# Kernel tuning notes

Measured on AMD Instinct MI355X. Metric: run time of the kernel, lower is better.

The kernel has to match this reference:

```python
import jax, jax.numpy as jnp
import numpy as np

HID, OUT, VOCAB, MSIZE, MDIM = 1024, 512, 1024, 262144, 128


def setup_inputs() -> dict:
    key = jax.random.key(0)
    ks = jax.random.split(key, 16)
    s = lambda i, shape, scale=0.02: jax.random.normal(ks[i], shape, dtype=jnp.float32) * scale
    return {
        "input": s(0, (1, 1, VOCAB), 1.0),
        "hidden0": s(1, (1, 1, HID), 1.0),
        "stack": s(2, (MSIZE, MDIM), 1.0),
        "W_ih": s(3, (HID, VOCAB)),
        "W_hh": s(4, (HID, HID)),
        "b_ih": s(5, (HID,)),
        "b_hh": s(6, (HID,)),
        "W_y": s(7, (OUT, HID)),
        "b_y": s(8, (OUT,)),
        "W_n": s(9, (MDIM, HID)),
        "b_n": s(10, (MDIM,)),
        "W_a": s(11, (2, HID)),
        "b_a": s(12, (2,)),
        "W_sh": s(13, (HID, MDIM)),
        "b_sh": s(14, (HID,)),
    }


def reference(input, hidden0, stack, W_ih, W_hh, b_ih, b_hh, W_y, b_y, W_n, b_n, W_a, b_a, W_sh, b_sh):
    # hidden_bar = W_sh(stack[0]).view(1,1,-1) + hidden0   -> (1,1,H)
    hidden_bar = (stack[0] @ W_sh.T + b_sh)[None, None, :] + hidden0
    # single-step, single-layer tanh RNN cell
    h = jnp.tanh(input @ W_ih.T + b_ih + hidden_bar @ W_hh.T + b_hh)  # (1,1,H)
    output = jax.nn.sigmoid(h @ W_y.T + b_y).reshape(-1, OUT)          # (1,OUT)
    action_weights = jax.nn.softmax(h @ W_a.T + b_a, axis=2).reshape(-1)  # (2,)
    new_elt = jax.nn.sigmoid(h @ W_n.T + b_n).reshape(1, MDIM)         # (1,MDIM)
    push_side = jnp.concatenate([new_elt, stack[:-1]], axis=0)
    pop_side = jnp.concatenate([stack[1:], jnp.zeros((1, MDIM), dtype=stack.dtype)], axis=0)
    new_stack = action_weights[0] * push_side + action_weights[1] * pop_side
    return output, h, new_stack
```

## Files before the change

### kernel.cpp

```cpp
#include <hip/hip_runtime.h>
#include <cmath>

#define HID 1024
#define OUTN 512
#define VOCABN 1024
#define MSIZE 262144
#define MDIM 128

#define WS_TIH 0
#define WS_HB  1024
#define WS_H   2048
#define WS_AW  3072
#define WS_NE  3076

typedef float f4_t __attribute__((ext_vector_type(4)));

__device__ __forceinline__ float wred(float v) {
#pragma unroll
    for (int m = 32; m; m >>= 1) v += __shfl_xor(v, m, 64);
    return v;
}

__device__ __forceinline__ float dot4(const float4* __restrict__ a,
                                      const float4* __restrict__ b,
                                      int n4, int lane) {
    float acc = 0.f;
    for (int k = lane; k < n4; k += 64) {
        float4 x = a[k], y = b[k];
        acc = fmaf(x.x, y.x, fmaf(x.y, y.y, fmaf(x.z, y.z, fmaf(x.w, y.w, acc))));
    }
    return wred(acc);
}

__global__ void k_pre(const float* __restrict__ input, const float* __restrict__ hidden0,
                      const float* __restrict__ stack, const float* __restrict__ W_ih,
                      const float* __restrict__ b_ih, const float* __restrict__ W_sh,
                      const float* __restrict__ b_sh, float* __restrict__ ws) {
    const int lane = threadIdx.x & 63;
    const int row = blockIdx.x * (blockDim.x >> 6) + (threadIdx.x >> 6);
    if (row >= HID) return;
    float t  = dot4((const float4*)(W_ih + row * VOCABN), (const float4*)input, VOCABN / 4, lane);
    float hb = dot4((const float4*)(W_sh + row * MDIM), (const float4*)stack, MDIM / 4, lane);
    if (lane == 0) {
        ws[WS_TIH + row] = t + b_ih[row];
        ws[WS_HB + row]  = hb + b_sh[row] + hidden0[row];
    }
}

__global__ void k_h(const float* __restrict__ W_hh, const float* __restrict__ b_hh,
                    float* __restrict__ ws, float* __restrict__ d_out) {
    const int lane = threadIdx.x & 63;
    const int row = blockIdx.x * (blockDim.x >> 6) + (threadIdx.x >> 6);
    if (row >= HID) return;
    float a = dot4((const float4*)(W_hh + row * HID), (const float4*)(ws + WS_HB), HID / 4, lane);
    if (lane == 0) {
        float h = tanhf(ws[WS_TIH + row] + a + b_hh[row]);
        ws[WS_H + row] = h;
        d_out[OUTN + row] = h;
    }
}

__global__ void k_heads(const float* __restrict__ W_y, const float* __restrict__ b_y,
                        const float* __restrict__ W_n, const float* __restrict__ b_n,
                        const float* __restrict__ W_a, const float* __restrict__ b_a,
                        float* __restrict__ ws, float* __restrict__ d_out) {
    const int lane = threadIdx.x & 63;
    const int row = blockIdx.x * (blockDim.x >> 6) + (threadIdx.x >> 6);
    const float4* h4 = (const float4*)(ws + WS_H);
    if (row < OUTN) {
        float a = dot4((const float4*)(W_y + row * HID), h4, HID / 4, lane);
        if (lane == 0) d_out[row] = 1.f / (1.f + expf(-(a + b_y[row])));
    } else if (row < OUTN + MDIM) {
        const int m = row - OUTN;
        float a = dot4((const float4*)(W_n + m * HID), h4, HID / 4, lane);
        if (lane == 0) ws[WS_NE + m] = 1.f / (1.f + expf(-(a + b_n[m])));
    } else if (row == OUTN + MDIM) {
        float l0 = dot4((const float4*)(W_a), h4, HID / 4, lane);
        float l1 = dot4((const float4*)(W_a + HID), h4, HID / 4, lane);
        if (lane == 0) {
            l0 += b_a[0];
            l1 += b_a[1];
            const float mx = fmaxf(l0, l1);
            const float e0 = expf(l0 - mx), e1 = expf(l1 - mx);
            const float s = e0 + e1;
            ws[WS_AW]     = e0 / s;
            ws[WS_AW + 1] = e1 / s;
        }
    }
}

__global__ __launch_bounds__(256, 8) void k_stack(
    const float* __restrict__ stack, const float* __restrict__ ws,
    float* __restrict__ out_stack) {
    const float aw0 = ws[WS_AW];
    const float aw1 = ws[WS_AW + 1];
    const float4* s4  = (const float4*)stack;
    const float4* ne4 = (const float4*)(ws + WS_NE);
    f4_t* o4 = (f4_t*)out_stack;
    const int total4 = MSIZE * (MDIM / 4);
    const int lane = threadIdx.x & 63;
    const int wid  = blockIdx.x * 4 + (threadIdx.x >> 6);
    const long base = (long)wid * 1024;

    float4 prev;
    if (wid == 0) prev = (lane < 32) ? ne4[lane] : s4[lane - 32];
    else          prev = s4[base - 32 + lane];

#pragma unroll 4
    for (int i = 0; i < 16; ++i) {
        const long A = base + i * 64;
        const long nidx = A + 32 + lane;
        float4 next = make_float4(0.f, 0.f, 0.f, 0.f);
        if (nidx < total4) next = s4[nidx];
        f4_t r;
        r.x = fmaf(aw0, prev.x, aw1 * next.x);
        r.y = fmaf(aw0, prev.y, aw1 * next.y);
        r.z = fmaf(aw0, prev.z, aw1 * next.z);
        r.w = fmaf(aw0, prev.w, aw1 * next.w);
        __builtin_nontemporal_store(r, &o4[A + lane]);
        prev = next;
    }
}

extern "C" void kernel_launch(void* const* d_in, const int* in_sizes, int n_in,
                              void* d_out, int out_size, void* d_ws, size_t ws_size,
                              hipStream_t stream) {
    const float* input   = (const float*)d_in[0];
    const float* hidden0 = (const float*)d_in[1];
    const float* stack   = (const float*)d_in[2];
    const float* W_ih    = (const float*)d_in[3];
    const float* W_hh    = (const float*)d_in[4];
    const float* b_ih    = (const float*)d_in[5];
    const float* b_hh    = (const float*)d_in[6];
    const float* W_y     = (const float*)d_in[7];
    const float* b_y     = (const float*)d_in[8];
    const float* W_n     = (const float*)d_in[9];
    const float* b_n     = (const float*)d_in[10];
    const float* W_a     = (const float*)d_in[11];
    const float* b_a     = (const float*)d_in[12];
    const float* W_sh    = (const float*)d_in[13];
    const float* b_sh    = (const float*)d_in[14];
    float* out = (float*)d_out;
    float* ws  = (float*)d_ws;

    k_pre<<<256, 256, 0, stream>>>(input, hidden0, stack, W_ih, b_ih, W_sh, b_sh, ws);
    k_h<<<256, 256, 0, stream>>>(W_hh, b_hh, ws, out);
    k_heads<<<161, 256, 0, stream>>>(W_y, b_y, W_n, b_n, W_a, b_a, ws, out);
    k_stack<<<2048, 256, 0, stream>>>(stack, ws, out + OUTN + HID);
}
```

Measured before the change: 60.09 us.

## Fuse RNN matvec chain into one cooperative kernel with grid syncs

Merges the three dependent matvec kernels (pre-activation, hidden update, output heads) into one cooperative kernel launched with 256 blocks. Grid-wide barriers replace the kernel boundaries between stages. The aim is to cut two launch gaps and kernel drain/fill overhead. In exchange it adds cooperative-launch overhead and grid-sync cost, and still needs a separate stack kernel.

Measured after the change: 118.0 us. 1.96x slower.

```diff
diff --git a/kernel.cpp b/kernel.cpp
--- a/kernel.cpp
+++ b/kernel.cpp
@@ -1,5 +1,8 @@
 #include <hip/hip_runtime.h>
+#include <hip/hip_cooperative_groups.h>
 #include <cmath>
+
+namespace cg = cooperative_groups;
 
 #define HID 1024
 #define OUTN 512
@@ -32,59 +35,64 @@
     return wred(acc);
 }
 
-__global__ void k_pre(const float* __restrict__ input, const float* __restrict__ hidden0,
-                      const float* __restrict__ stack, const float* __restrict__ W_ih,
-                      const float* __restrict__ b_ih, const float* __restrict__ W_sh,
-                      const float* __restrict__ b_sh, float* __restrict__ ws) {
+__global__ __launch_bounds__(256) void k_chain(
+    const float* __restrict__ input, const float* __restrict__ hidden0,
+    const float* __restrict__ stack, const float* __restrict__ W_ih,
+    const float* __restrict__ b_ih, const float* __restrict__ W_hh,
+    const float* __restrict__ b_hh, const float* __restrict__ W_y,
+    const float* __restrict__ b_y, const float* __restrict__ W_n,
+    const float* __restrict__ b_n, const float* __restrict__ W_a,
+    const float* __restrict__ b_a, const float* __restrict__ W_sh,
+    const float* __restrict__ b_sh, float* __restrict__ ws,
+    float* __restrict__ d_out) {
+    cg::grid_group grid = cg::this_grid();
     const int lane = threadIdx.x & 63;
-    const int row = blockIdx.x * (blockDim.x >> 6) + (threadIdx.x >> 6);
-    if (row >= HID) return;
-    float t  = dot4((const float4*)(W_ih + row * VOCABN), (const float4*)input, VOCABN / 4, lane);
-    float hb = dot4((const float4*)(W_sh + row * MDIM), (const float4*)stack, MDIM / 4, lane);
-    if (lane == 0) {
-        ws[WS_TIH + row] = t + b_ih[row];
-        ws[WS_HB + row]  = hb + b_sh[row] + hidden0[row];
+    const int row  = blockIdx.x * 4 + (threadIdx.x >> 6);
+
+    {
+        const float t  = dot4((const float4*)(W_ih + row * VOCABN),
+                              (const float4*)input, VOCABN / 4, lane);
+        const float hb = dot4((const float4*)(W_sh + row * MDIM),
+                              (const float4*)stack, MDIM / 4, lane);
+        if (lane == 0) {
+            ws[WS_TIH + row] = t + b_ih[row];
+            ws[WS_HB + row]  = hb + b_sh[row] + hidden0[row];
+        }
     }
-}
+    grid.sync();
 
-__global__ void k_h(const float* __restrict__ W_hh, const float* __restrict__ b_hh,
-                    float* __restrict__ ws, float* __restrict__ d_out) {
-    const int lane = threadIdx.x & 63;
-    const int row = blockIdx.x * (blockDim.x >> 6) + (threadIdx.x >> 6);
-    if (row >= HID) return;
-    float a = dot4((const float4*)(W_hh + row * HID), (const float4*)(ws + WS_HB), HID / 4, lane);
-    if (lane == 0) {
-        float h = tanhf(ws[WS_TIH + row] + a + b_hh[row]);
-        ws[WS_H + row] = h;
-        d_out[OUTN + row] = h;
+    {
+        const float a = dot4((const float4*)(W_hh + row * HID),
+                             (const float4*)(ws + WS_HB), HID / 4, lane);
+        if (lane == 0) {
+            const float h = tanhf(ws[WS_TIH + row] + a + b_hh[row]);
+            ws[WS_H + row] = h;
+            d_out[OUTN + row] = h;
+        }
     }
-}
+    grid.sync();
 
-__global__ void k_heads(const float* __restrict__ W_y, const float* __restrict__ b_y,
-                        const float* __restrict__ W_n, const float* __restrict__ b_n,
-                        const float* __restrict__ W_a, const float* __restrict__ b_a,
-                        float* __restrict__ ws, float* __restrict__ d_out) {
-    const int lane = threadIdx.x & 63;
-    const int row = blockIdx.x * (blockDim.x >> 6) + (threadIdx.x >> 6);
-    const float4* h4 = (const float4*)(ws + WS_H);
-    if (row < OUTN) {
-        float a = dot4((const float4*)(W_y + row * HID), h4, HID / 4, lane);
-        if (lane == 0) d_out[row] = 1.f / (1.f + expf(-(a + b_y[row])));
-    } else if (row < OUTN + MDIM) {
-        const int m = row - OUTN;
-        float a = dot4((const float4*)(W_n + m * HID), h4, HID / 4, lane);
-        if (lane == 0) ws[WS_NE + m] = 1.f / (1.f + expf(-(a + b_n[m])));
-    } else if (row == OUTN + MDIM) {
-        float l0 = dot4((const float4*)(W_a), h4, HID / 4, lane);
-        float l1 = dot4((const float4*)(W_a + HID), h4, HID / 4, lane);
-        if (lane == 0) {
-            l0 += b_a[0];
-            l1 += b_a[1];
-            const float mx = fmaxf(l0, l1);
-            const float e0 = expf(l0 - mx), e1 = expf(l1 - mx);
-            const float s = e0 + e1;
-            ws[WS_AW]     = e0 / s;
-            ws[WS_AW + 1] = e1 / s;
+    {
+        const float4* h4 = (const float4*)(ws + WS_H);
+        if (row < OUTN) {
+            const float a = dot4((const float4*)(W_y + row * HID), h4, HID / 4, lane);
+            if (lane == 0) d_out[row] = 1.f / (1.f + expf(-(a + b_y[row])));
+        } else if (row < OUTN + MDIM) {
+            const int m = row - OUTN;
+            const float a = dot4((const float4*)(W_n + m * HID), h4, HID / 4, lane);
+            if (lane == 0) ws[WS_NE + m] = 1.f / (1.f + expf(-(a + b_n[m])));
+        } else if (row == OUTN + MDIM) {
+            float l0 = dot4((const float4*)(W_a), h4, HID / 4, lane);
+            float l1 = dot4((const float4*)(W_a + HID), h4, HID / 4, lane);
+            if (lane == 0) {
+                l0 += b_a[0];
+                l1 += b_a[1];
+                const float mx = fmaxf(l0, l1);
+                const float e0 = expf(l0 - mx), e1 = expf(l1 - mx);
+                const float s = e0 + e1;
+                ws[WS_AW]     = e0 / s;
+                ws[WS_AW + 1] = e1 / s;
+            }
         }
     }
 }
@@ -143,8 +151,12 @@
     float* out = (float*)d_out;
     float* ws  = (float*)d_ws;
 
-    k_pre<<<256, 256, 0, stream>>>(input, hidden0, stack, W_ih, b_ih, W_sh, b_sh, ws);
-    k_h<<<256, 256, 0, stream>>>(W_hh, b_hh, ws, out);
-    k_heads<<<161, 256, 0, stream>>>(W_y, b_y, W_n, b_n, W_a, b_a, ws, out);
+    void* args[] = {
+        (void*)&input, (void*)&hidden0, (void*)&stack, (void*)&W_ih,
+        (void*)&b_ih, (void*)&W_hh, (void*)&b_hh, (void*)&W_y,
+        (void*)&b_y, (void*)&W_n, (void*)&b_n, (void*)&W_a,
+        (void*)&b_a, (void*)&W_sh, (void*)&b_sh, (void*)&ws, (void*)&out,
+    };
+    hipLaunchCooperativeKernel((void*)k_chain, dim3(256), dim3(256), args, 0, stream);
     k_stack<<<2048, 256, 0, stream>>>(stack, ws, out + OUTN + HID);
 }
```
